# Kernel optimization log

Measured on AMD Instinct MI355X. Metric: run time of the kernel, lower is better.

Reference implementation:

```python
import jax, jax.numpy as jnp
import numpy as np

B, NIN, L, N, K, NOUT = 4096, 512, 16, 512, 32, 256
TOTAL = NIN + L * N  # 8704 total nodes in the DAG


def setup_inputs() -> dict:
    key = jax.random.key(0)
    ks = jax.random.split(key, 5)
    x = jax.random.normal(ks[0], (B, NIN), jnp.float32)
    W = jax.random.normal(ks[1], (L, N, K), jnp.float32) * 0.2
    b = jax.random.normal(ks[2], (L, N), jnp.float32) * 0.1
    W_out = jax.random.normal(ks[3], (NOUT, K), jnp.float32) * 0.2
    b_out = jax.random.normal(ks[4], (NOUT,), jnp.float32) * 0.1
    rng = np.random.default_rng(0)
    # layer l may only read nodes computed before it (topological validity)
    idx = np.stack([rng.integers(0, NIN + l * N, size=(N, K)) for l in range(L)]).astype(np.int32)
    idx_out = rng.integers(0, TOTAL, size=(NOUT, K)).astype(np.int32)
    return {"x": x, "W": W, "b": b, "W_out": W_out, "b_out": b_out,
            "idx": jnp.asarray(idx), "idx_out": jnp.asarray(idx_out)}


def reference(x, W, b, W_out, b_out, idx, idx_out):
    # buffer of all node activations, filled topologically (out_dict analog)
    buf0 = jnp.zeros((B, TOTAL), x.dtype).at[:, :NIN].set(x)

    def step(carry, layer):
        buf, l = carry
        li, lW, lb = layer
        gathered = buf[:, li]  # [B, N, K] irregular gather of predecessor outputs
        out = jax.nn.sigmoid(jnp.einsum('bnk,nk->bn', gathered, lW) + lb)  # per-node tiny linear + sigmoid
        buf = jax.lax.dynamic_update_slice(buf, out, (0, NIN + l * N))
        return (buf, l + 1), None

    (buf, _), _ = jax.lax.scan(step, (buf0, jnp.int32(0)), (idx, W, b))
    g = buf[:, idx_out]  # [B, NOUT, K]
    return jax.nn.sigmoid(jnp.einsum('bok,ok->bo', g, W_out) + b_out)
```

## Files before the change

kernel.cpp:

```cpp
#include <hip/hip_runtime.h>
#include <hip/hip_fp16.h>
#include <math.h>

#define B     4096
#define NIN   512
#define L     16
#define N     512
#define K     32
#define NOUT  256
#define HID   (L * N)
#define TOTAL (NIN + L * N)
#define BROWS 4
#define BLOCK 512

typedef __attribute__((ext_vector_type(2))) _Float16 hv2;
typedef __attribute__((ext_vector_type(8))) _Float16 h8;
typedef __attribute__((ext_vector_type(8))) unsigned short u16x8;

struct alignas(8) hh { hv2 lo, hi; };

__device__ __forceinline__ float sigmoidf_fast(float z) {
    return 1.0f / (1.0f + __expf(-z));
}

__global__ void repack_kernel(const float* __restrict__ W,
                              const int*   __restrict__ idx,
                              const float* __restrict__ W_out,
                              const int*   __restrict__ idx_out,
                              _Float16* __restrict__ wh,
                              unsigned short* __restrict__ i16,
                              _Float16* __restrict__ who,
                              unsigned short* __restrict__ io16)
{
    const int n = blockIdx.x * 64 + threadIdx.x;
    const int* ip; const float* wp; _Float16* wo; unsigned short* io; int scale;
    if (n < HID) {
        ip = idx + (size_t)n * K;      wp = W + (size_t)n * K;
        wo = wh + (size_t)n * K;       io = i16 + (size_t)n * K;   scale = 3;
    } else if (n < HID + NOUT) {
        const int m = n - HID;
        ip = idx_out + (size_t)m * K;  wp = W_out + (size_t)m * K;
        wo = who + (size_t)m * K;      io = io16 + (size_t)m * K;  scale = 0;
    } else {
        return;
    }
    const int rot = n & 15;

    int ci[K]; float cw[K];
#pragma unroll
    for (int j = 0; j < K; ++j) { ci[j] = ip[j]; cw[j] = wp[j]; }

    unsigned long long r0 = 0, r1 = 0;
    int sl[K];
    unsigned used = 0;
#pragma unroll
    for (int j = 0; j < K; ++j) {
        const int key = ci[j] & 15;
        const int sh  = (key & 7) << 3;
        int rank;
        if (key < 8) { rank = (int)((r0 >> sh) & 0xff); r0 += 1ull << sh; }
        else         { rank = (int)((r1 >> sh) & 0xff); r1 += 1ull << sh; }
        if (rank < 2) {
            const int s = ((key - rot) & 15) + (rank << 4);
            sl[j] = s; used |= 1u << s;
        } else {
            sl[j] = -1;
        }
    }
#pragma unroll
    for (int j = 0; j < K; ++j) {
        int s = sl[j];
        if (s < 0) { s = (int)__builtin_ctz(~used); used |= 1u << s; }
        io[s] = (unsigned short)(ci[j] << scale);
        wo[s] = (_Float16)cw[j];
    }
}

#define GROUP8(CI, W8, SH, ACC)                                               \
    {                                                                         \
        hv2 aL = {(_Float16)0.f, (_Float16)0.f};                              \
        hv2 aH = {(_Float16)0.f, (_Float16)0.f};                              \
        _Pragma("unroll")                                                     \
        for (int j = 0; j < 8; ++j) {                                         \
            const int c = ((int)(CI)[j]) << (SH);                             \
            const hh  v = *(const hh*)((const char*)buf + c);                 \
            hv2 wt2; wt2.x = (W8)[j]; wt2.y = (W8)[j];                        \
            aL = __builtin_elementwise_fma(v.lo, wt2, aL);                    \
            aH = __builtin_elementwise_fma(v.hi, wt2, aH);                    \
        }                                                                     \
        ACC.x += (float)aL.x;  ACC.y += (float)aL.y;                          \
        ACC.z += (float)aH.x;  ACC.w += (float)aH.y;                          \
    }

#define LAYER(IDXQ, LI)                                                       \
    {                                                                         \
        const h8* wp = (const h8*)(wh + ((size_t)(LI) * N + t) * K);          \
        const h8 w0 = wp[0], w1 = wp[1], w2 = wp[2], w3 = wp[3];              \
        float4 acc = make_float4(0.f, 0.f, 0.f, 0.f);                         \
        GROUP8(IDXQ[0], w0, 0, acc)                                           \
        GROUP8(IDXQ[1], w1, 0, acc)                                           \
        GROUP8(IDXQ[2], w2, 0, acc)                                           \
        GROUP8(IDXQ[3], w3, 0, acc)                                           \
        const float bb = bias[(LI) * N + t];                                  \
        hh o;                                                                 \
        o.lo.x = (_Float16)sigmoidf_fast(acc.x + bb);                         \
        o.lo.y = (_Float16)sigmoidf_fast(acc.y + bb);                         \
        o.hi.x = (_Float16)sigmoidf_fast(acc.z + bb);                         \
        o.hi.y = (_Float16)sigmoidf_fast(acc.w + bb);                         \
        buf[NIN + (LI) * N + t] = o;                                          \
    }

__global__ __launch_bounds__(BLOCK, 4)
void ffnet_kernel(const float* __restrict__ x,
                  const float* __restrict__ bias,
                  const float* __restrict__ bias_out,
                  const _Float16*       __restrict__ wh,
                  const unsigned short* __restrict__ i16,
                  const _Float16*       __restrict__ who,
                  const unsigned short* __restrict__ io16,
                  float* __restrict__ out)
{
    __shared__ hh buf[TOTAL];

    const int t  = threadIdx.x;
    const int r0 = blockIdx.x * BROWS;

    {
        hh v;
        v.lo.x = (_Float16)x[(size_t)(r0 + 0) * NIN + t];
        v.lo.y = (_Float16)x[(size_t)(r0 + 1) * NIN + t];
        v.hi.x = (_Float16)x[(size_t)(r0 + 2) * NIN + t];
        v.hi.y = (_Float16)x[(size_t)(r0 + 3) * NIN + t];
        buf[t] = v;
    }

    u16x8 ia[4], ib[4];
    {
        const u16x8* ip = (const u16x8*)(i16 + (size_t)t * K);
        ia[0] = ip[0]; ia[1] = ip[1]; ia[2] = ip[2]; ia[3] = ip[3];
    }
    __syncthreads();

    for (int l = 0; l < L; l += 2) {
        {
            const u16x8* np = (const u16x8*)(i16 + ((size_t)(l + 1) * N + t) * K);
            ib[0] = np[0]; ib[1] = np[1]; ib[2] = np[2]; ib[3] = np[3];
        }
        LAYER(ia, l)
        __syncthreads();

        if (l + 2 < L) {
            const u16x8* np = (const u16x8*)(i16 + ((size_t)(l + 2) * N + t) * K);
            ia[0] = np[0]; ia[1] = np[1]; ia[2] = np[2]; ia[3] = np[3];
        } else if (t < NOUT) {
            const u16x8* np = (const u16x8*)(io16 + (size_t)t * K);
            ia[0] = np[0]; ia[1] = np[1]; ia[2] = np[2]; ia[3] = np[3];
        }
        LAYER(ib, l + 1)
        __syncthreads();
    }

    if (t < NOUT) {
        const h8* wp = (const h8*)(who + (size_t)t * K);
        const h8 w0 = wp[0], w1 = wp[1], w2 = wp[2], w3 = wp[3];

        float4 acc = make_float4(0.f, 0.f, 0.f, 0.f);
        GROUP8(ia[0], w0, 3, acc)
        GROUP8(ia[1], w1, 3, acc)
        GROUP8(ia[2], w2, 3, acc)
        GROUP8(ia[3], w3, 3, acc)

        const float bb = bias_out[t];
        out[(size_t)(r0 + 0) * NOUT + t] = sigmoidf_fast(acc.x + bb);
        out[(size_t)(r0 + 1) * NOUT + t] = sigmoidf_fast(acc.y + bb);
        out[(size_t)(r0 + 2) * NOUT + t] = sigmoidf_fast(acc.z + bb);
        out[(size_t)(r0 + 3) * NOUT + t] = sigmoidf_fast(acc.w + bb);
    }
}

extern "C" void kernel_launch(void* const* d_in, const int* in_sizes, int n_in,
                              void* d_out, int out_size, void* d_ws, size_t ws_size,
                              hipStream_t stream) {
    const float* x     = (const float*)d_in[0];
    const float* W     = (const float*)d_in[1];
    const float* b     = (const float*)d_in[2];
    const float* W_out = (const float*)d_in[3];
    const float* b_out = (const float*)d_in[4];
    const int*   idx   = (const int*)d_in[5];
    const int*   idx_o = (const int*)d_in[6];
    float* out = (float*)d_out;

    char* ws = (char*)d_ws;
    _Float16*       wh   = (_Float16*)      (ws);
    unsigned short* i16  = (unsigned short*)(ws + 524288);
    _Float16*       who  = (_Float16*)      (ws + 1048576);
    unsigned short* io16 = (unsigned short*)(ws + 1048576 + 16384);

    const int nneur = HID + NOUT;
    repack_kernel<<<dim3((nneur + 63) / 64), dim3(64), 0, stream>>>(
        W, idx, W_out, idx_o, wh, i16, who, io16);

    ffnet_kernel<<<dim3(B / BROWS), dim3(BLOCK), 0, stream>>>(
        x, b, b_out, wh, i16, who, io16, out);
}
```

Baseline: 147.0 us.

## Halve batch rows per block to shrink LDS buffer and raise occupancy

After: 201.9 us. +37.3%, slower.

```diff
diff --git a/kernel.cpp b/kernel.cpp
--- a/kernel.cpp
+++ b/kernel.cpp
@@ -10,14 +10,12 @@
 #define NOUT  256
 #define HID   (L * N)
 #define TOTAL (NIN + L * N)
-#define BROWS 4
+#define BROWS 2
 #define BLOCK 512
 
 typedef __attribute__((ext_vector_type(2))) _Float16 hv2;
 typedef __attribute__((ext_vector_type(8))) _Float16 h8;
 typedef __attribute__((ext_vector_type(8))) unsigned short u16x8;
-
-struct alignas(8) hh { hv2 lo, hi; };
 
 __device__ __forceinline__ float sigmoidf_fast(float z) {
     return 1.0f / (1.0f + __expf(-z));
@@ -33,35 +31,42 @@
                               unsigned short* __restrict__ io16)
 {
     const int n = blockIdx.x * 64 + threadIdx.x;
-    const int* ip; const float* wp; _Float16* wo; unsigned short* io; int scale;
+    const int* ip; const float* wp; _Float16* wo; unsigned short* io;
     if (n < HID) {
         ip = idx + (size_t)n * K;      wp = W + (size_t)n * K;
-        wo = wh + (size_t)n * K;       io = i16 + (size_t)n * K;   scale = 3;
+        wo = wh + (size_t)n * K;       io = i16 + (size_t)n * K;
     } else if (n < HID + NOUT) {
         const int m = n - HID;
         ip = idx_out + (size_t)m * K;  wp = W_out + (size_t)m * K;
-        wo = who + (size_t)m * K;      io = io16 + (size_t)m * K;  scale = 0;
+        wo = who + (size_t)m * K;      io = io16 + (size_t)m * K;
     } else {
         return;
     }
-    const int rot = n & 15;
+    const int rot = n & 31;
 
     int ci[K]; float cw[K];
+    {
+        const int4*   ip4 = (const int4*)ip;
+        const float4* wp4 = (const float4*)wp;
 #pragma unroll
-    for (int j = 0; j < K; ++j) { ci[j] = ip[j]; cw[j] = wp[j]; }
-
-    unsigned long long r0 = 0, r1 = 0;
+        for (int q = 0; q < 8; ++q) {
+            const int4   a = ip4[q];
+            const float4 f = wp4[q];
+            ci[q * 4 + 0] = a.x; ci[q * 4 + 1] = a.y;
+            ci[q * 4 + 2] = a.z; ci[q * 4 + 3] = a.w;
+            cw[q * 4 + 0] = f.x; cw[q * 4 + 1] = f.y;
+            cw[q * 4 + 2] = f.z; cw[q * 4 + 3] = f.w;
+        }
+    }
+
+    unsigned seen = 0, used = 0;
     int sl[K];
-    unsigned used = 0;
 #pragma unroll
     for (int j = 0; j < K; ++j) {
-        const int key = ci[j] & 15;
-        const int sh  = (key & 7) << 3;
-        int rank;
-        if (key < 8) { rank = (int)((r0 >> sh) & 0xff); r0 += 1ull << sh; }
-        else         { rank = (int)((r1 >> sh) & 0xff); r1 += 1ull << sh; }
-        if (rank < 2) {
-            const int s = ((key - rot) & 15) + (rank << 4);
+        const int key = ci[j] & 31;
+        if (!((seen >> key) & 1u)) {
+            seen |= 1u << key;
+            const int s = (key - rot) & 31;
             sl[j] = s; used |= 1u << s;
         } else {
             sl[j] = -1;
@@ -71,46 +76,41 @@
     for (int j = 0; j < K; ++j) {
         int s = sl[j];
         if (s < 0) { s = (int)__builtin_ctz(~used); used |= 1u << s; }
-        io[s] = (unsigned short)(ci[j] << scale);
+        io[s] = (unsigned short)(ci[j] << 2);
         wo[s] = (_Float16)cw[j];
     }
 }
 
-#define GROUP8(CI, W8, SH, ACC)                                               \
+#define GROUP8(CI, W8, AX, AY)                                                \
     {                                                                         \
         hv2 aL = {(_Float16)0.f, (_Float16)0.f};                              \
-        hv2 aH = {(_Float16)0.f, (_Float16)0.f};                              \
         _Pragma("unroll")                                                     \
         for (int j = 0; j < 8; ++j) {                                         \
-            const int c = ((int)(CI)[j]) << (SH);                             \
-            const hh  v = *(const hh*)((const char*)buf + c);                 \
+            const int c = (int)(CI)[j];                                       \
+            const hv2 v = *(const hv2*)((const char*)buf + c);                \
             hv2 wt2; wt2.x = (W8)[j]; wt2.y = (W8)[j];                        \
-            aL = __builtin_elementwise_fma(v.lo, wt2, aL);                    \
-            aH = __builtin_elementwise_fma(v.hi, wt2, aH);                    \
+            aL = __builtin_elementwise_fma(v, wt2, aL);                       \
         }                                                                     \
-        ACC.x += (float)aL.x;  ACC.y += (float)aL.y;                          \
-        ACC.z += (float)aH.x;  ACC.w += (float)aH.y;                          \
+        AX += (float)aL.x;  AY += (float)aL.y;                                \
     }
 
 #define LAYER(IDXQ, LI)                                                       \
     {                                                                         \
         const h8* wp = (const h8*)(wh + ((size_t)(LI) * N + t) * K);          \
         const h8 w0 = wp[0], w1 = wp[1], w2 = wp[2], w3 = wp[3];              \
-        float4 acc = make_float4(0.f, 0.f, 0.f, 0.f);                         \
-        GROUP8(IDXQ[0], w0, 0, acc)                                           \
-        GROUP8(IDXQ[1], w1, 0, acc)                                           \
-        GROUP8(IDXQ[2], w2, 0, acc)                                           \
-        GROUP8(IDXQ[3], w3, 0, acc)                                           \
+        float ax = 0.f, ay = 0.f;                                             \
+        GROUP8(IDXQ[0], w0, ax, ay)                                           \
+        GROUP8(IDXQ[1], w1, ax, ay)                                           \
+        GROUP8(IDXQ[2], w2, ax, ay)                                           \
+        GROUP8(IDXQ[3], w3, ax, ay)                                           \
         const float bb = bias[(LI) * N + t];                                  \
-        hh o;                                                                 \
-        o.lo.x = (_Float16)sigmoidf_fast(acc.x + bb);                         \
-        o.lo.y = (_Float16)sigmoidf_fast(acc.y + bb);                         \
-        o.hi.x = (_Float16)sigmoidf_fast(acc.z + bb);                         \
-        o.hi.y = (_Float16)sigmoidf_fast(acc.w + bb);                         \
+        hv2 o;                                                                \
+        o.x = (_Float16)sigmoidf_fast(ax + bb);                               \
+        o.y = (_Float16)sigmoidf_fast(ay + bb);                               \
         buf[NIN + (LI) * N + t] = o;                                          \
     }
 
-__global__ __launch_bounds__(BLOCK, 4)
+__global__ __launch_bounds__(BLOCK, 8)
 void ffnet_kernel(const float* __restrict__ x,
                   const float* __restrict__ bias,
                   const float* __restrict__ bias_out,
@@ -120,17 +120,15 @@
                   const unsigned short* __restrict__ io16,
                   float* __restrict__ out)
 {
-    __shared__ hh buf[TOTAL];
+    __shared__ hv2 buf[TOTAL];
 
     const int t  = threadIdx.x;
     const int r0 = blockIdx.x * BROWS;
 
     {
-        hh v;
-        v.lo.x = (_Float16)x[(size_t)(r0 + 0) * NIN + t];
-        v.lo.y = (_Float16)x[(size_t)(r0 + 1) * NIN + t];
-        v.hi.x = (_Float16)x[(size_t)(r0 + 2) * NIN + t];
-        v.hi.y = (_Float16)x[(size_t)(r0 + 3) * NIN + t];
+        hv2 v;
+        v.x = (_Float16)x[(size_t)(r0 + 0) * NIN + t];
+        v.y = (_Float16)x[(size_t)(r0 + 1) * NIN + t];
         buf[t] = v;
     }
 
@@ -164,17 +162,15 @@
         const h8* wp = (const h8*)(who + (size_t)t * K);
         const h8 w0 = wp[0], w1 = wp[1], w2 = wp[2], w3 = wp[3];
 
-        float4 acc = make_float4(0.f, 0.f, 0.f, 0.f);
-        GROUP8(ia[0], w0, 3, acc)
-        GROUP8(ia[1], w1, 3, acc)
-        GROUP8(ia[2], w2, 3, acc)
-        GROUP8(ia[3], w3, 3, acc)
+        float ax = 0.f, ay = 0.f;
+        GROUP8(ia[0], w0, ax, ay)
+        GROUP8(ia[1], w1, ax, ay)
+        GROUP8(ia[2], w2, ax, ay)
+        GROUP8(ia[3], w3, ax, ay)
 
         const float bb = bias_out[t];
-        out[(size_t)(r0 + 0) * NOUT + t] = sigmoidf_fast(acc.x + bb);
-        out[(size_t)(r0 + 1) * NOUT + t] = sigmoidf_fast(acc.y + bb);
-        out[(size_t)(r0 + 2) * NOUT + t] = sigmoidf_fast(acc.z + bb);
-        out[(size_t)(r0 + 3) * NOUT + t] = sigmoidf_fast(acc.w + bb);
+        out[(size_t)(r0 + 0) * NOUT + t] = sigmoidf_fast(ax + bb);
+        out[(size_t)(r0 + 1) * NOUT + t] = sigmoidf_fast(ay + bb);
     }
 }
 
```
